# Kernel tuning notes

Measured on AMD Instinct MI355X. Metric: run time of the kernel, lower is better.

Reference implementation:

```python
import jax, jax.numpy as jnp
import numpy as np

WINDOW = 4
EPS = 1e-5


def setup_inputs() -> dict:
    key = jax.random.key(0)
    ks = jax.random.split(key, 12)
    B, T, D = 2, 4096, 1024
    H = D // 2
    s = 0.02
    return {
        "x": jax.random.normal(ks[0], (B, T, D), dtype=jnp.float32),
        # tension_net: Linear(2D -> D/2), SiLU, Linear(D/2 -> 1). Weights stored [in, out].
        "w1": jax.random.normal(ks[1], (2 * D, H), dtype=jnp.float32) * s,
        "b1": jnp.zeros((H,), dtype=jnp.float32),
        "w2": jax.random.normal(ks[2], (H, 1), dtype=jnp.float32) * s,
        "b2": jnp.zeros((1,), dtype=jnp.float32),
        # wv: Linear(D -> D)
        "wv_w": jax.random.normal(ks[3], (D, D), dtype=jnp.float32) * s,
        "wv_b": jnp.zeros((D,), dtype=jnp.float32),
        # merge: Linear(2D -> D)
        "merge_w": jax.random.normal(ks[4], (2 * D, D), dtype=jnp.float32) * s,
        "merge_b": jnp.zeros((D,), dtype=jnp.float32),
        # LayerNorm(D)
        "gamma": jnp.ones((D,), dtype=jnp.float32),
        "beta": jnp.zeros((D,), dtype=jnp.float32),
    }


def reference(x, w1, b1, w2, b2, wv_w, wv_b, merge_w, merge_b, gamma, beta):
    B, T, D = x.shape
    W = WINDOW
    # Causal sliding-window neighbor gather: nb[:, t, w] = x[:, t-w-1] if t-w-1 >= 0 else 0.
    idx = jnp.arange(T)[:, None] - jnp.arange(W)[None, :] - 1          # [T, W]
    valid = (idx >= 0)                                                  # [T, W]
    nb = jnp.take(x, jnp.clip(idx, 0, None), axis=1)                   # [B, T, W, D]
    nb = jnp.where(valid[None, :, :, None], nb, jnp.zeros((), x.dtype))
    # Pairwise tension gate: tiny MLP on [h_t, nb].
    h_t = jnp.broadcast_to(x[:, :, None, :], (B, T, W, D))
    pair = jnp.concatenate([h_t, nb], axis=-1)                          # [B, T, W, 2D]
    hid = jax.nn.silu(jnp.einsum('btwe,eh->btwh', pair, w1) + b1)       # [B, T, W, D/2]
    tau = jax.nn.sigmoid((jnp.einsum('btwh,ho->btwo', hid, w2) + b2)[..., 0])  # [B, T, W]
    # Value projection of neighbors (note: zero-padded neighbors still get wv bias, matching torch).
    v = jnp.einsum('btwd,de->btwe', nb, wv_w) + wv_b                    # [B, T, W, D]
    msg = jnp.einsum('btw,btwd->btd', tau, v)                           # [B, T, D]
    # Merge + LayerNorm.
    y = jnp.einsum('bte,ed->btd', jnp.concatenate([x, msg], axis=-1), merge_w) + merge_b
    mu = jnp.mean(y, axis=-1, keepdims=True)
    var = jnp.mean(jnp.square(y - mu), axis=-1, keepdims=True)
    y = (y - mu) * jax.lax.rsqrt(var + EPS) * gamma + beta
    return y
```

## Files before the change

### kernel.cpp

```cpp
#include <hip/hip_runtime.h>
#include <hip/hip_bf16.h>

#define TT 4096
#define TD 1024
#define TM 8192
#define CN 3072
#define EPS 1e-5f

typedef __bf16 bf16;
typedef __bf16 bf16x2 __attribute__((ext_vector_type(2)));
typedef __bf16 bf16x4 __attribute__((ext_vector_type(4)));
typedef __bf16 bf16x8 __attribute__((ext_vector_type(8)));
typedef float  f32x4  __attribute__((ext_vector_type(4)));

#define GLOBAL_AS __attribute__((address_space(1)))
#define LDS_AS    __attribute__((address_space(3)))

__global__ __launch_bounds__(256) void prep_kernel(const float* __restrict__ x,
                                                   const float* __restrict__ w1,
                                                   const float* __restrict__ wv_w,
                                                   const float* __restrict__ wv_b,
                                                   const float* __restrict__ merge_w,
                                                   bf16* __restrict__ Xbf,
                                                   bf16* __restrict__ BigBT,
                                                   bf16* __restrict__ Amb,
                                                   bf16* __restrict__ WvBf,
                                                   float* __restrict__ cvec) {
    __shared__ float tile[32][33];
    int b = blockIdx.x;
    const int tid = threadIdx.x;

    if (b < 4) {
        int j = b * 256 + tid;
        const float* col = merge_w + (size_t)1024 * 1024 + j;
        float acc = 0.f;
#pragma unroll 16
        for (int e = 0; e < 1024; ++e) acc += wv_b[e] * col[(size_t)e * 1024];
        cvec[j] = acc;
        return;
    }
    b -= 4;
    if (b < 8192) {
        int i = b * 256 + tid;
        float4 v = ((const float4*)x)[i];
        bf16x4 o; o[0] = (bf16)v.x; o[1] = (bf16)v.y; o[2] = (bf16)v.z; o[3] = (bf16)v.w;
        *(bf16x4*)(Xbf + (size_t)i * 4) = o;
        return;
    }
    b -= 8192;

    const float* src; bf16* dst; int srcN, tilesX, dstOff;
    if (b < 512)       {           src = w1;                        srcN = 512;  tilesX = 16; dst = BigBT; dstOff = 0;    }
    else if (b < 1024) { b -= 512; src = w1 + (size_t)1024 * 512;   srcN = 512;  tilesX = 16; dst = BigBT; dstOff = 512;  }
    else if (b < 2048) { b -= 1024; src = merge_w;                  srcN = 1024; tilesX = 32; dst = BigBT; dstOff = 2048; }
    else if (b < 3072) { b -= 2048; src = merge_w + (size_t)1024 * 1024; srcN = 1024; tilesX = 32; dst = Amb; dstOff = 0; }
    else {
        b -= 3072;
        int i = b * 256 + tid;
        float4 v = ((const float4*)wv_w)[i];
        bf16x4 o; o[0] = (bf16)v.x; o[1] = (bf16)v.y; o[2] = (bf16)v.z; o[3] = (bf16)v.w;
        *(bf16x4*)(WvBf + (size_t)i * 4) = o;
        return;
    }
    int n0 = (b % tilesX) * 32, k0 = (b / tilesX) * 32;
    int tx = tid & 31, ty = tid >> 5;
#pragma unroll
    for (int r = 0; r < 32; r += 8)
        tile[ty + r][tx] = src[(size_t)(k0 + ty + r) * srcN + n0 + tx];
    __syncthreads();
#pragma unroll
    for (int r = 0; r < 32; r += 8)
        dst[(size_t)(dstOff + n0 + ty + r) * 1024 + k0 + tx] = (bf16)tile[tx][ty + r];
}

template <typename OutT, bool SWIZ>
__global__ __launch_bounds__(256) void gemm_bt(const bf16* __restrict__ A, int lda,
                                               const bf16* __restrict__ BT,
                                               OutT* __restrict__ C, int N, int K) {
    __shared__ bf16 As[128 * 64];
    __shared__ bf16 Bs[128 * 64];
    int bx = blockIdx.x, by = blockIdx.y;
    if (SWIZ) {
        int L = by * gridDim.x + bx;
        int xcd = L & 7, idx = L >> 3;
        int nyx = gridDim.y >> 3;
        by = xcd * nyx + idx / gridDim.x;
        bx = idx % gridDim.x;
    }
    const int m0 = by * 128;
    const int n0 = bx * 128;
    const int tid = threadIdx.x;
    const int wave = tid >> 6, lane = tid & 63;
    const int wr = (wave >> 1) * 64, wc = (wave & 1) * 64;
    const int lrow = lane & 15, cbase = lane >> 4;
    const int sw = lrow & 7;

    f32x4 acc[4][4] = {};

    for (int k0 = 0; k0 < K; k0 += 64) {
        __syncthreads();
#pragma unroll
        for (int c = 0; c < 4; ++c) {
            int e = (c * 256 + tid) * 8;
            int row = e >> 6;
            int q = (e >> 3) & 7;
            int gcol = ((q ^ (row & 7)) << 3);
            const bf16* ga = A  + (size_t)(m0 + row) * lda + k0 + gcol;
            const bf16* gb = BT + (size_t)(n0 + row) * K   + k0 + gcol;
            __builtin_amdgcn_global_load_lds((const GLOBAL_AS void*)ga,
                                             (LDS_AS void*)(As + e), 16, 0, 0);
            __builtin_amdgcn_global_load_lds((const GLOBAL_AS void*)gb,
                                             (LDS_AS void*)(Bs + e), 16, 0, 0);
        }
        __syncthreads();

#pragma unroll
        for (int kk = 0; kk < 2; ++kk) {
            const int qo = ((cbase + kk * 4) ^ sw) << 3;
            bf16x8 af[4], bfr[4];
#pragma unroll
            for (int i = 0; i < 4; ++i) {
                af[i]  = *(const bf16x8*)(As + (wr + i * 16 + lrow) * 64 + qo);
                bfr[i] = *(const bf16x8*)(Bs + (wc + i * 16 + lrow) * 64 + qo);
            }
#pragma unroll
            for (int i = 0; i < 4; ++i)
#pragma unroll
                for (int j = 0; j < 4; ++j)
                    acc[i][j] = __builtin_amdgcn_mfma_f32_16x16x32_bf16(af[i], bfr[j], acc[i][j], 0, 0, 0);
        }
    }

    const int lr = (lane >> 4) * 4, lc = lane & 15;
#pragma unroll
    for (int i = 0; i < 4; ++i)
#pragma unroll
        for (int j = 0; j < 4; ++j)
#pragma unroll
            for (int r = 0; r < 4; ++r)
                C[(size_t)(m0 + wr + i * 16 + lr + r) * N + (n0 + wc + j * 16 + lc)]
                    = (OutT)acc[i][j][r];
}

__global__ __launch_bounds__(256) void final_kernel(const bf16* __restrict__ C,
                                                    const float* __restrict__ b1,
                                                    const float* __restrict__ b2,
                                                    const float* __restrict__ w2,
                                                    const float* __restrict__ cvec,
                                                    const float* __restrict__ merge_b,
                                                    const float* __restrict__ gamma,
                                                    const float* __restrict__ beta,
                                                    float* __restrict__ out) {
    const int row = blockIdx.x;
    const int t = row & (TT - 1);
    const int tid = threadIdx.x;
    const bf16* Crow = C + (size_t)row * CN;

    const int h = tid * 2;
    bf16x2 u2 = *(const bf16x2*)(Crow + h);
    float2 b1v = *(const float2*)(b1 + h);
    float2 w2v = *(const float2*)(w2 + h);
    const float u0 = (float)u2[0] + b1v.x;
    const float u1 = (float)u2[1] + b1v.y;

    float partial[4];
#pragma unroll
    for (int w = 0; w < 4; ++w) {
        float vn0 = 0.f, vn1 = 0.f;
        if (t >= w + 1) {
            bf16x2 v2 = *(const bf16x2*)(C + (size_t)(row - w - 1) * CN + 512 + h);
            vn0 = (float)v2[0]; vn1 = (float)v2[1];
        }
        float z0 = u0 + vn0, z1 = u1 + vn1;
        float h0 = z0 / (1.f + __expf(-z0));
        float h1 = z1 / (1.f + __expf(-z1));
        partial[w] = h0 * w2v.x + h1 * w2v.y;
    }
#pragma unroll
    for (int w = 0; w < 4; ++w)
        for (int off = 32; off; off >>= 1)
            partial[w] += __shfl_down(partial[w], off, 64);

    __shared__ float red[4][4];
    __shared__ float staus[4];
    const int lane = tid & 63, wave = tid >> 6;
    if (lane == 0)
#pragma unroll
        for (int w = 0; w < 4; ++w) red[w][wave] = partial[w];
    __syncthreads();
    if (tid < 4) {
        float s = red[tid][0] + red[tid][1] + red[tid][2] + red[tid][3] + b2[0];
        staus[tid] = 1.f / (1.f + __expf(-s));
    }
    __syncthreads();
    const float tau0 = staus[0], tau1 = staus[1], tau2 = staus[2], tau3 = staus[3];
    const float tsum = tau0 + tau1 + tau2 + tau3;
    const float taus[4] = {tau0, tau1, tau2, tau3};

    const int d0 = tid * 4;
    bf16x4 y1 = *(const bf16x4*)(Crow + 2048 + d0);
    float4 cv = *(const float4*)(cvec + d0);
    float4 mb = *(const float4*)(merge_b + d0);
    float v[4] = {(float)y1[0] + tsum * cv.x + mb.x,
                  (float)y1[1] + tsum * cv.y + mb.y,
                  (float)y1[2] + tsum * cv.z + mb.z,
                  (float)y1[3] + tsum * cv.w + mb.w};
#pragma unroll
    for (int w = 0; w < 4; ++w) {
        if (t >= w + 1) {
            bf16x4 p = *(const bf16x4*)(C + (size_t)(row - w - 1) * CN + 1024 + d0);
#pragma unroll
            for (int j = 0; j < 4; ++j) v[j] += taus[w] * (float)p[j];
        }
    }

    float s = v[0] + v[1] + v[2] + v[3];
    float ss = v[0]*v[0] + v[1]*v[1] + v[2]*v[2] + v[3]*v[3];
    for (int off = 32; off; off >>= 1) {
        s  += __shfl_down(s, off, 64);
        ss += __shfl_down(ss, off, 64);
    }
    __shared__ float rs[4], rss[4];
    __shared__ float smu, srstd;
    if (lane == 0) { rs[wave] = s; rss[wave] = ss; }
    __syncthreads();
    if (tid == 0) {
        float S = rs[0] + rs[1] + rs[2] + rs[3];
        float SS = rss[0] + rss[1] + rss[2] + rss[3];
        float mu = S * (1.f / TD);
        float var = SS * (1.f / TD) - mu * mu;
        smu = mu; srstd = rsqrtf(var + EPS);
    }
    __syncthreads();
    const float mu = smu, r = srstd;
    float4 g  = *(const float4*)(gamma + d0);
    float4 bt = *(const float4*)(beta + d0);
    float4 o;
    o.x = (v[0] - mu) * r * g.x + bt.x;
    o.y = (v[1] - mu) * r * g.y + bt.y;
    o.z = (v[2] - mu) * r * g.z + bt.z;
    o.w = (v[3] - mu) * r * g.w + bt.w;
    *(float4*)(out + (size_t)row * TD + d0) = o;
}

extern "C" void kernel_launch(void* const* d_in, const int* in_sizes, int n_in,
                              void* d_out, int out_size, void* d_ws, size_t ws_size,
                              hipStream_t stream) {
    const float* x       = (const float*)d_in[0];
    const float* w1      = (const float*)d_in[1];
    const float* b1      = (const float*)d_in[2];
    const float* w2      = (const float*)d_in[3];
    const float* b2      = (const float*)d_in[4];
    const float* wv_w    = (const float*)d_in[5];
    const float* wv_b    = (const float*)d_in[6];
    const float* merge_w = (const float*)d_in[7];
    const float* merge_b = (const float*)d_in[8];
    const float* gamma   = (const float*)d_in[9];
    const float* beta    = (const float*)d_in[10];
    float* out = (float*)d_out;

    char* ws = (char*)d_ws;
    bf16*  Xbf   = (bf16*)ws;  ws += (size_t)TM * 1024 * 2;
    bf16*  BigBT = (bf16*)ws;  ws += (size_t)CN * 1024 * 2;
    bf16*  Amb   = (bf16*)ws;  ws += (size_t)1024 * 1024 * 2;
    bf16*  WvBf  = (bf16*)ws;  ws += (size_t)1024 * 1024 * 2;
    float* cvec  = (float*)ws; ws += (size_t)1024 * 4;
    bf16*  Cbuf  = (bf16*)ws;

    prep_kernel<<<12292, 256, 0, stream>>>(x, w1, wv_w, wv_b, merge_w,
                                           Xbf, BigBT, Amb, WvBf, cvec);

    gemm_bt<bf16, false><<<dim3(8, 8), 256, 0, stream>>>(
        Amb, 1024, WvBf, BigBT + (size_t)1024 * 1024, 1024, 1024);

    gemm_bt<bf16, true><<<dim3(CN / 128, TM / 128), 256, 0, stream>>>(
        Xbf, 1024, BigBT, Cbuf, CN, 1024);

    final_kernel<<<TM, 256, 0, stream>>>(Cbuf, b1, b2, w2, cvec, merge_b,
                                         gamma, beta, out);
}
```

Before: 242.1 us.

## Split cvec reduction, use small-tile weight GEMM, one-wave-per-row final kernel

The serial 1024-length cvec dot product is split into four partial sums across 16 blocks, and a new wprime kernel reduces them. The same kernel computes the merge·Wv product with 64x64 tiles on 256 blocks instead of 64 blocks of 128x128, so more CUs are busy. The final kernel now handles one row per wave with xor-shuffle reductions, which removes the LDS and __syncthreads round trips. In exchange it adds a partials buffer, and each lane now holds 16 values, which raises register pressure.

```diff
diff --git a/kernel.cpp b/kernel.cpp
--- a/kernel.cpp
+++ b/kernel.cpp
@@ -8,7 +8,6 @@
 #define EPS 1e-5f
 
 typedef __bf16 bf16;
-typedef __bf16 bf16x2 __attribute__((ext_vector_type(2)));
 typedef __bf16 bf16x4 __attribute__((ext_vector_type(4)));
 typedef __bf16 bf16x8 __attribute__((ext_vector_type(8)));
 typedef float  f32x4  __attribute__((ext_vector_type(4)));
@@ -25,21 +24,22 @@
                                                    bf16* __restrict__ BigBT,
                                                    bf16* __restrict__ Amb,
                                                    bf16* __restrict__ WvBf,
-                                                   float* __restrict__ cvec) {
+                                                   float* __restrict__ cvecP) {
     __shared__ float tile[32][33];
     int b = blockIdx.x;
     const int tid = threadIdx.x;
 
-    if (b < 4) {
-        int j = b * 256 + tid;
-        const float* col = merge_w + (size_t)1024 * 1024 + j;
+    if (b < 16) {
+        const int j = (b & 3) * 256 + tid;
+        const int e0 = (b >> 2) * 256;
+        const float* col = merge_w + (size_t)(1024 + e0) * 1024 + j;
         float acc = 0.f;
-#pragma unroll 16
-        for (int e = 0; e < 1024; ++e) acc += wv_b[e] * col[(size_t)e * 1024];
-        cvec[j] = acc;
+#pragma unroll 32
+        for (int e = 0; e < 256; ++e) acc += wv_b[e0 + e] * col[(size_t)e * 1024];
+        cvecP[(b >> 2) * 1024 + j] = acc;
         return;
     }
-    b -= 4;
+    b -= 16;
     if (b < 8192) {
         int i = b * 256 + tid;
         float4 v = ((const float4*)x)[i];
@@ -50,9 +50,9 @@
     b -= 8192;
 
     const float* src; bf16* dst; int srcN, tilesX, dstOff;
-    if (b < 512)       {           src = w1;                        srcN = 512;  tilesX = 16; dst = BigBT; dstOff = 0;    }
-    else if (b < 1024) { b -= 512; src = w1 + (size_t)1024 * 512;   srcN = 512;  tilesX = 16; dst = BigBT; dstOff = 512;  }
-    else if (b < 2048) { b -= 1024; src = merge_w;                  srcN = 1024; tilesX = 32; dst = BigBT; dstOff = 2048; }
+    if (b < 512)       {            src = w1;                        srcN = 512;  tilesX = 16; dst = BigBT; dstOff = 0;    }
+    else if (b < 1024) { b -= 512;  src = w1 + (size_t)1024 * 512;   srcN = 512;  tilesX = 16; dst = BigBT; dstOff = 512;  }
+    else if (b < 2048) { b -= 1024; src = merge_w;                   srcN = 1024; tilesX = 32; dst = BigBT; dstOff = 2048; }
     else if (b < 3072) { b -= 2048; src = merge_w + (size_t)1024 * 1024; srcN = 1024; tilesX = 32; dst = Amb; dstOff = 0; }
     else {
         b -= 3072;
@@ -73,10 +73,84 @@
         dst[(size_t)(dstOff + n0 + ty + r) * 1024 + k0 + tx] = (bf16)tile[tx][ty + r];
 }
 
-template <typename OutT, bool SWIZ>
+__global__ __launch_bounds__(256) void wprime_kernel(const bf16* __restrict__ Amb,
+                                                     const bf16* __restrict__ WvBf,
+                                                     bf16* __restrict__ Wout,
+                                                     const float* __restrict__ cvecP,
+                                                     float* __restrict__ cvec) {
+    int b = blockIdx.x;
+    if (b == 256) {
+        int j = threadIdx.x * 4;
+        float4 s0 = *(const float4*)(cvecP + j);
+        float4 s1 = *(const float4*)(cvecP + 1024 + j);
+        float4 s2 = *(const float4*)(cvecP + 2048 + j);
+        float4 s3 = *(const float4*)(cvecP + 3072 + j);
+        float4 o = {s0.x + s1.x + s2.x + s3.x, s0.y + s1.y + s2.y + s3.y,
+                    s0.z + s1.z + s2.z + s3.z, s0.w + s1.w + s2.w + s3.w};
+        *(float4*)(cvec + j) = o;
+        return;
+    }
+    __shared__ bf16 As[64 * 64];
+    __shared__ bf16 Bs[64 * 64];
+    const int m0 = (b >> 4) * 64;
+    const int n0 = (b & 15) * 64;
+    const int tid = threadIdx.x;
+    const int wave = tid >> 6, lane = tid & 63;
+    const int wr = (wave >> 1) * 32, wc = (wave & 1) * 32;
+    const int lrow = lane & 15, cbase = lane >> 4;
+    const int sw = lrow & 7;
+
+    f32x4 acc[2][2] = {};
+
+    for (int k0 = 0; k0 < 1024; k0 += 64) {
+        __syncthreads();
+#pragma unroll
+        for (int c = 0; c < 2; ++c) {
+            int e = (c * 256 + tid) * 8;
+            int row = e >> 6;
+            int q = (e >> 3) & 7;
+            int gcol = ((q ^ (row & 7)) << 3);
+            const bf16* ga = Amb  + (size_t)(m0 + row) * 1024 + k0 + gcol;
+            const bf16* gb = WvBf + (size_t)(n0 + row) * 1024 + k0 + gcol;
+            __builtin_amdgcn_global_load_lds((const GLOBAL_AS void*)ga,
+                                             (LDS_AS void*)(As + e), 16, 0, 0);
+            __builtin_amdgcn_global_load_lds((const GLOBAL_AS void*)gb,
+                                             (LDS_AS void*)(Bs + e), 16, 0, 0);
+        }
+        __syncthreads();
+
+#pragma unroll
+        for (int kk = 0; kk < 2; ++kk) {
+            const int qo = ((cbase + kk * 4) ^ sw) << 3;
+            bf16x8 af[2], bfr[2];
+#pragma unroll
+            for (int i = 0; i < 2; ++i) {
+                af[i]  = *(const bf16x8*)(As + (wr + i * 16 + lrow) * 64 + qo);
+                bfr[i] = *(const bf16x8*)(Bs + (wc + i * 16 + lrow) * 64 + qo);
+            }
+#pragma unroll
+            for (int i = 0; i < 2; ++i)
+#pragma unroll
+                for (int j = 0; j < 2; ++j)
+                    acc[i][j] = __builtin_amdgcn_mfma_f32_16x16x32_bf16(af[i], bfr[j], acc[i][j], 0, 0, 0);
+        }
+    }
+
+    const int lr = (lane >> 4) * 4, lc = lane & 15;
+#pragma unroll
+    for (int i = 0; i < 2; ++i)
+#pragma unroll
+        for (int j = 0; j < 2; ++j)
+#pragma unroll
+            for (int r = 0; r < 4; ++r)
+                Wout[(size_t)(m0 + wr + i * 16 + lr + r) * 1024 + (n0 + wc + j * 16 + lc)]
+                    = (bf16)acc[i][j][r];
+}
+
+template <bool SWIZ>
 __global__ __launch_bounds__(256) void gemm_bt(const bf16* __restrict__ A, int lda,
                                                const bf16* __restrict__ BT,
-                                               OutT* __restrict__ C, int N, int K) {
+                                               bf16* __restrict__ C, int N, int K) {
     __shared__ bf16 As[128 * 64];
     __shared__ bf16 Bs[128 * 64];
     int bx = blockIdx.x, by = blockIdx.y;
@@ -139,7 +213,7 @@
 #pragma unroll
             for (int r = 0; r < 4; ++r)
                 C[(size_t)(m0 + wr + i * 16 + lr + r) * N + (n0 + wc + j * 16 + lc)]
-                    = (OutT)acc[i][j][r];
+                    = (bf16)acc[i][j][r];
 }
 
 __global__ __launch_bounds__(256) void final_kernel(const bf16* __restrict__ C,
@@ -151,96 +225,104 @@
                                                     const float* __restrict__ gamma,
                                                     const float* __restrict__ beta,
                                                     float* __restrict__ out) {
-    const int row = blockIdx.x;
+    const int wave = threadIdx.x >> 6, lane = threadIdx.x & 63;
+    const int row = blockIdx.x * 4 + wave;
     const int t = row & (TT - 1);
-    const int tid = threadIdx.x;
     const bf16* Crow = C + (size_t)row * CN;
 
-    const int h = tid * 2;
-    bf16x2 u2 = *(const bf16x2*)(Crow + h);
-    float2 b1v = *(const float2*)(b1 + h);
-    float2 w2v = *(const float2*)(w2 + h);
-    const float u0 = (float)u2[0] + b1v.x;
-    const float u1 = (float)u2[1] + b1v.y;
+    const int h0 = lane * 8;
+    bf16x8 u8 = *(const bf16x8*)(Crow + h0);
+    float4 b1a = *(const float4*)(b1 + h0), b1b = *(const float4*)(b1 + h0 + 4);
+    float4 w2a = *(const float4*)(w2 + h0), w2b = *(const float4*)(w2 + h0 + 4);
+    float u[8] = {(float)u8[0] + b1a.x, (float)u8[1] + b1a.y,
+                  (float)u8[2] + b1a.z, (float)u8[3] + b1a.w,
+                  (float)u8[4] + b1b.x, (float)u8[5] + b1b.y,
+                  (float)u8[6] + b1b.z, (float)u8[7] + b1b.w};
+    const float w2v[8] = {w2a.x, w2a.y, w2a.z, w2a.w, w2b.x, w2b.y, w2b.z, w2b.w};
 
     float partial[4];
 #pragma unroll
     for (int w = 0; w < 4; ++w) {
-        float vn0 = 0.f, vn1 = 0.f;
+        float p = 0.f;
         if (t >= w + 1) {
-            bf16x2 v2 = *(const bf16x2*)(C + (size_t)(row - w - 1) * CN + 512 + h);
-            vn0 = (float)v2[0]; vn1 = (float)v2[1];
-        }
-        float z0 = u0 + vn0, z1 = u1 + vn1;
-        float h0 = z0 / (1.f + __expf(-z0));
-        float h1 = z1 / (1.f + __expf(-z1));
-        partial[w] = h0 * w2v.x + h1 * w2v.y;
+            bf16x8 v8 = *(const bf16x8*)(C + (size_t)(row - w - 1) * CN + 512 + h0);
+#pragma unroll
+            for (int k = 0; k < 8; ++k) {
+                float z = u[k] + (float)v8[k];
+                p += (z / (1.f + __expf(-z))) * w2v[k];
+            }
+        } else {
+#pragma unroll
+            for (int k = 0; k < 8; ++k) {
+                float z = u[k];
+                p += (z / (1.f + __expf(-z))) * w2v[k];
+            }
+        }
+        partial[w] = p;
     }
 #pragma unroll
     for (int w = 0; w < 4; ++w)
-        for (int off = 32; off; off >>= 1)
-            partial[w] += __shfl_down(partial[w], off, 64);
-
-    __shared__ float red[4][4];
-    __shared__ float staus[4];
-    const int lane = tid & 63, wave = tid >> 6;
-    if (lane == 0)
-#pragma unroll
-        for (int w = 0; w < 4; ++w) red[w][wave] = partial[w];
-    __syncthreads();
-    if (tid < 4) {
-        float s = red[tid][0] + red[tid][1] + red[tid][2] + red[tid][3] + b2[0];
-        staus[tid] = 1.f / (1.f + __expf(-s));
-    }
-    __syncthreads();
-    const float tau0 = staus[0], tau1 = staus[1], tau2 = staus[2], tau3 = staus[3];
-    const float tsum = tau0 + tau1 + tau2 + tau3;
-    const float taus[4] = {tau0, tau1, tau2, tau3};
-
-    const int d0 = tid * 4;
-    bf16x4 y1 = *(const bf16x4*)(Crow + 2048 + d0);
-    float4 cv = *(const float4*)(cvec + d0);
-    float4 mb = *(const float4*)(merge_b + d0);
-    float v[4] = {(float)y1[0] + tsum * cv.x + mb.x,
-                  (float)y1[1] + tsum * cv.y + mb.y,
-                  (float)y1[2] + tsum * cv.z + mb.z,
-                  (float)y1[3] + tsum * cv.w + mb.w};
+#pragma unroll
+        for (int off = 1; off < 64; off <<= 1)
+            partial[w] += __shfl_xor(partial[w], off, 64);
+
+    const float bias2 = b2[0];
+    float taus[4];
+#pragma unroll
+    for (int w = 0; w < 4; ++w)
+        taus[w] = 1.f / (1.f + __expf(-(partial[w] + bias2)));
+    const float tsum = taus[0] + taus[1] + taus[2] + taus[3];
+
+    const int d0 = lane * 16;
+    bf16x8 y1a = *(const bf16x8*)(Crow + 2048 + d0);
+    bf16x8 y1b = *(const bf16x8*)(Crow + 2048 + d0 + 8);
+    float v[16];
+#pragma unroll
+    for (int k = 0; k < 8; ++k) { v[k] = (float)y1a[k]; v[8 + k] = (float)y1b[k]; }
+#pragma unroll
+    for (int q = 0; q < 4; ++q) {
+        float4 cv = *(const float4*)(cvec + d0 + q * 4);
+        float4 mb = *(const float4*)(merge_b + d0 + q * 4);
+        v[q*4+0] += tsum * cv.x + mb.x; v[q*4+1] += tsum * cv.y + mb.y;
+        v[q*4+2] += tsum * cv.z + mb.z; v[q*4+3] += tsum * cv.w + mb.w;
+    }
 #pragma unroll
     for (int w = 0; w < 4; ++w) {
         if (t >= w + 1) {
-            bf16x4 p = *(const bf16x4*)(C + (size_t)(row - w - 1) * CN + 1024 + d0);
-#pragma unroll
-            for (int j = 0; j < 4; ++j) v[j] += taus[w] * (float)p[j];
-        }
-    }
-
-    float s = v[0] + v[1] + v[2] + v[3];
-    float ss = v[0]*v[0] + v[1]*v[1] + v[2]*v[2] + v[3]*v[3];
-    for (int off = 32; off; off >>= 1) {
-        s  += __shfl_down(s, off, 64);
-        ss += __shfl_down(ss, off, 64);
-    }
-    __shared__ float rs[4], rss[4];
-    __shared__ float smu, srstd;
-    if (lane == 0) { rs[wave] = s; rss[wave] = ss; }
-    __syncthreads();
-    if (tid == 0) {
-        float S = rs[0] + rs[1] + rs[2] + rs[3];
-        float SS = rss[0] + rss[1] + rss[2] + rss[3];
-        float mu = S * (1.f / TD);
-        float var = SS * (1.f / TD) - mu * mu;
-        smu = mu; srstd = rsqrtf(var + EPS);
-    }
-    __syncthreads();
-    const float mu = smu, r = srstd;
-    float4 g  = *(const float4*)(gamma + d0);
-    float4 bt = *(const float4*)(beta + d0);
-    float4 o;
-    o.x = (v[0] - mu) * r * g.x + bt.x;
-    o.y = (v[1] - mu) * r * g.y + bt.y;
-    o.z = (v[2] - mu) * r * g.z + bt.z;
-    o.w = (v[3] - mu) * r * g.w + bt.w;
-    *(float4*)(out + (size_t)row * TD + d0) = o;
+            const bf16* Pn = C + (size_t)(row - w - 1) * CN + 1024 + d0;
+            bf16x8 pa = *(const bf16x8*)Pn;
+            bf16x8 pb = *(const bf16x8*)(Pn + 8);
+#pragma unroll
+            for (int k = 0; k < 8; ++k) {
+                v[k] += taus[w] * (float)pa[k];
+                v[8 + k] += taus[w] * (float)pb[k];
+            }
+        }
+    }
+
+    float s = 0.f, ss = 0.f;
+#pragma unroll
+    for (int k = 0; k < 16; ++k) { s += v[k]; ss += v[k] * v[k]; }
+#pragma unroll
+    for (int off = 1; off < 64; off <<= 1) {
+        s  += __shfl_xor(s, off, 64);
+        ss += __shfl_xor(ss, off, 64);
+    }
+    const float mu = s * (1.f / TD);
+    const float var = ss * (1.f / TD) - mu * mu;
+    const float r = rsqrtf(var + EPS);
+
+#pragma unroll
+    for (int q = 0; q < 4; ++q) {
+        float4 g  = *(const float4*)(gamma + d0 + q * 4);
+        float4 bt = *(const float4*)(beta + d0 + q * 4);
+        float4 o;
+        o.x = (v[q*4+0] - mu) * r * g.x + bt.x;
+        o.y = (v[q*4+1] - mu) * r * g.y + bt.y;
+        o.z = (v[q*4+2] - mu) * r * g.z + bt.z;
+        o.w = (v[q*4+3] - mu) * r * g.w + bt.w;
+        *(float4*)(out + (size_t)row * TD + d0 + q * 4) = o;
+    }
 }
 
 extern "C" void kernel_launch(void* const* d_in, const int* in_sizes, int n_in,
@@ -264,18 +346,19 @@
     bf16*  BigBT = (bf16*)ws;  ws += (size_t)CN * 1024 * 2;
     bf16*  Amb   = (bf16*)ws;  ws += (size_t)1024 * 1024 * 2;
     bf16*  WvBf  = (bf16*)ws;  ws += (size_t)1024 * 1024 * 2;
+    float* cvecP = (float*)ws; ws += (size_t)4 * 1024 * 4;
     float* cvec  = (float*)ws; ws += (size_t)1024 * 4;
     bf16*  Cbuf  = (bf16*)ws;
 
-    prep_kernel<<<12292, 256, 0, stream>>>(x, w1, wv_w, wv_b, merge_w,
-                                           Xbf, BigBT, Amb, WvBf, cvec);
-
-    gemm_bt<bf16, false><<<dim3(8, 8), 256, 0, stream>>>(
-        Amb, 1024, WvBf, BigBT + (size_t)1024 * 1024, 1024, 1024);
-
-    gemm_bt<bf16, true><<<dim3(CN / 128, TM / 128), 256, 0, stream>>>(
+    prep_kernel<<<12304, 256, 0, stream>>>(x, w1, wv_w, wv_b, merge_w,
+                                           Xbf, BigBT, Amb, WvBf, cvecP);
+
+    wprime_kernel<<<257, 256, 0, stream>>>(Amb, WvBf, BigBT + (size_t)1024 * 1024,
+                                           cvecP, cvec);
+
+    gemm_bt<true><<<dim3(CN / 128, TM / 128), 256, 0, stream>>>(
         Xbf, 1024, BigBT, Cbuf, CN, 1024);
 
-    final_kernel<<<TM, 256, 0, stream>>>(Cbuf, b1, b2, w2, cvec, merge_b,
-                                         gamma, beta, out);
-}
+    final_kernel<<<TM / 4, 256, 0, stream>>>(Cbuf, b1, b2, w2, cvec, merge_b,
+                                             gamma, beta, out);
+}
```

New measurement: 202.2 us. -16.5%, faster.
